# Kernel optimization log

Hardware: AMD Instinct MI355X
Metric: run time of the kernel (lower is better)

Reference implementation:

```python
import jax, jax.numpy as jnp
import numpy as np

B, T, D, H = 128, 256, 1024, 1024


def setup_inputs() -> dict:
    key = jax.random.key(0)
    ks = jax.random.split(key, 6)
    s = 0.02
    return {
        "x": jax.random.normal(ks[0], (B, T, D), dtype=jnp.float32),
        "mask": jnp.ones((B, T), dtype=jnp.float32),
        "Wi_f": jax.random.normal(ks[1], (3 * H, D), dtype=jnp.float32) * s,
        "Wh_f": jax.random.normal(ks[2], (3 * H, H), dtype=jnp.float32) * s,
        "bi_f": jnp.zeros((3 * H,), dtype=jnp.float32),
        "bh_f": jnp.zeros((3 * H,), dtype=jnp.float32),
        "Wi_r": jax.random.normal(ks[3], (3 * H, D), dtype=jnp.float32) * s,
        "Wh_r": jax.random.normal(ks[4], (3 * H, H), dtype=jnp.float32) * s,
        "bi_r": jnp.zeros((3 * H,), dtype=jnp.float32),
        "bh_r": jnp.zeros((3 * H,), dtype=jnp.float32),
    }


def _gru_scan(x_tbd, m_tb, Wi, Wh, bi, bh):
    # x_tbd: [T,B,D], m_tb: [T,B]; returns all hidden states [T,B,H]
    h0 = jnp.zeros((x_tbd.shape[1], Wh.shape[1]), dtype=x_tbd.dtype)

    def step(h, inp):
        x_t, m_t = inp
        gi = x_t @ Wi.T + bi          # [B,3H]
        gh = h @ Wh.T + bh            # [B,3H]
        i_r, i_z, i_n = jnp.split(gi, 3, axis=-1)
        h_r, h_z, h_n = jnp.split(gh, 3, axis=-1)
        r = jax.nn.sigmoid(i_r + h_r)
        z = jax.nn.sigmoid(i_z + h_z)
        n = jnp.tanh(i_n + r * h_n)
        h_new = (1.0 - z) * n + z * h
        m = m_t[:, None]
        h_out = m * h_new + (1.0 - m) * h  # masked carry-over
        return h_out, h_out

    _, hs = jax.lax.scan(step, h0, (x_tbd, m_tb))
    return hs


def reference(x, mask, Wi_f, Wh_f, bi_f, bh_f, Wi_r, Wh_r, bi_r, bh_r):
    x_t = jnp.transpose(x, (1, 0, 2))   # [T,B,D]
    m_t = jnp.transpose(mask, (1, 0))   # [T,B]
    hs_f = _gru_scan(x_t, m_t, Wi_f, Wh_f, bi_f, bh_f)              # forward in time
    hs_r = _gru_scan(x_t[::-1], m_t[::-1], Wi_r, Wh_r, bi_r, bh_r)  # reverse in time
    hs_r = hs_r[::-1]
    out = jnp.concatenate([hs_f, hs_r], axis=-1)  # [T,B,2H]
    return jnp.transpose(out, (1, 0, 2))          # [B,T,2H]
```

## Files before the change

kernel.cpp:

```cpp
#include <hip/hip_runtime.h>
#include <hip/hip_bf16.h>

typedef __hip_bfloat16 bf16;
typedef __attribute__((ext_vector_type(8))) short bf16x8;
typedef __attribute__((ext_vector_type(4))) float f32x4;

#define GLDS16(g, l)                                                  \
  __builtin_amdgcn_global_load_lds(                                   \
      (const __attribute__((address_space(1))) void*)(g),             \
      (__attribute__((address_space(3))) void*)(l), 16, 0, 0)

__device__ __forceinline__ float bf2f(bf16 v) { return __bfloat162float(v); }
__device__ __forceinline__ short f2bf(float f) {
  bf16 b = __float2bfloat16(f);
  return *reinterpret_cast<short*>(&b);
}

__device__ __forceinline__ unsigned long long ald64(const void* p) {
  return __hip_atomic_load((const unsigned long long*)p, __ATOMIC_RELAXED,
                           __HIP_MEMORY_SCOPE_AGENT);
}
__device__ __forceinline__ void ast32(void* p, unsigned v) {
  __hip_atomic_store((unsigned*)p, v, __ATOMIC_RELAXED,
                     __HIP_MEMORY_SCOPE_AGENT);
}
__device__ __forceinline__ unsigned ald32(const void* p) {
  return __hip_atomic_load((const unsigned*)p, __ATOMIC_RELAXED,
                           __HIP_MEMORY_SCOPE_AGENT);
}

__global__ __launch_bounds__(256) void cvt_bf16(const float* __restrict__ in,
                                                bf16* __restrict__ out, int n) {
  const int i = (blockIdx.x * 256 + threadIdx.x) * 8;
  if (i >= n) return;
  const float4 u = *(const float4*)(in + i);
  const float4 v = *(const float4*)(in + i + 4);
  bf16x8 w;
  w[0] = f2bf(u.x); w[1] = f2bf(u.y); w[2] = f2bf(u.z); w[3] = f2bf(u.w);
  w[4] = f2bf(v.x); w[5] = f2bf(v.y); w[6] = f2bf(v.z); w[7] = f2bf(v.w);
  *(bf16x8*)(out + i) = w;
}

__global__ __launch_bounds__(256) void cvt_whb(const float* __restrict__ Wh_f,
                                               const float* __restrict__ Wh_r,
                                               bf16* __restrict__ Whb) {
  const int t = blockIdx.x * 256 + threadIdx.x;
  const int d = t / 393216;
  int r = t % 393216;
  const int cg = r / 6144;  r %= 6144;
  const int g = r / 2048;   r %= 2048;
  const int kk = r / 64;
  const int lane = r & 63;
  const float* Wh = d ? Wh_r : Wh_f;
  const int row = g * 1024 + cg * 16 + (lane & 15);
  const int col = kk * 32 + (lane >> 4) * 8;
  const float* s = Wh + (size_t)row * 1024 + col;
  const float4 u = *(const float4*)s;
  const float4 v = *(const float4*)(s + 4);
  bf16x8 w;
  w[0] = f2bf(u.x); w[1] = f2bf(u.y); w[2] = f2bf(u.z); w[3] = f2bf(u.w);
  w[4] = f2bf(v.x); w[5] = f2bf(v.y); w[6] = f2bf(v.z); w[7] = f2bf(v.w);
  *(bf16x8*)(Whb + (size_t)t * 8) = w;
}

__global__ __launch_bounds__(256) void gi_gemm(const bf16* __restrict__ X,
                                               const bf16* __restrict__ Wi,
                                               const float* __restrict__ bi,
                                               bf16* __restrict__ Gi) {
  __shared__ bf16 As[128 * 32];
  __shared__ bf16 Bs[128 * 32];
  const int tid = threadIdx.x;
  const int lane = tid & 63;
  const int w = tid >> 6;
  const int wm = w >> 1, wn = w & 1;
  const int m0 = blockIdx.y * 128;
  const int n0 = blockIdx.x * 128;
  const int rA = lane & 15;
  const int kl = (lane >> 4) * 8;

  f32x4 acc[4][4] = {};

  const bf16* Ab = X + (size_t)m0 * 1024;
  const bf16* Bb = Wi + (size_t)n0 * 1024;

  const int arow = tid >> 2;
  const int akk = (tid & 3) * 8;

  for (int kt = 0; kt < 1024; kt += 32) {
#pragma unroll
    for (int i = 0; i < 2; ++i) {
      GLDS16(Ab + (size_t)(i * 64 + arow) * 1024 + kt + akk,
             As + (i * 256 + w * 64) * 8);
      GLDS16(Bb + (size_t)(i * 64 + arow) * 1024 + kt + akk,
             Bs + (i * 256 + w * 64) * 8);
    }
    asm volatile("s_waitcnt vmcnt(0)" ::: "memory");
    __syncthreads();

    bf16x8 a[4], b[4];
#pragma unroll
    for (int f = 0; f < 4; ++f) {
      a[f] = *(const bf16x8*)(As + (wm * 64 + f * 16 + rA) * 32 + kl);
      b[f] = *(const bf16x8*)(Bs + (wn * 64 + f * 16 + rA) * 32 + kl);
    }
#pragma unroll
    for (int mf = 0; mf < 4; ++mf)
#pragma unroll
      for (int nf = 0; nf < 4; ++nf)
        acc[mf][nf] = __builtin_amdgcn_mfma_f32_16x16x32_bf16(
            a[mf], b[nf], acc[mf][nf], 0, 0, 0);
    __syncthreads();
  }

  const int rgrp = (lane >> 4) * 4;
#pragma unroll
  for (int nf = 0; nf < 4; ++nf) {
    const int col = n0 + wn * 64 + nf * 16 + rA;
    const float bv = bi[col];
#pragma unroll
    for (int mf = 0; mf < 4; ++mf) {
#pragma unroll
      for (int j = 0; j < 4; ++j) {
        const int row = m0 + wm * 64 + mf * 16 + rgrp + j;
        Gi[(size_t)row * 3072 + col] = __float2bfloat16(acc[mf][nf][j] + bv);
      }
    }
  }
}

__global__ __launch_bounds__(256, 1) void gru_persist_s(
    const bf16* __restrict__ Whb, const float* __restrict__ bh_f,
    const float* __restrict__ bh_r, const bf16* __restrict__ Gi,
    const float* __restrict__ mask, bf16* __restrict__ h16,
    unsigned* __restrict__ flags, float* __restrict__ out) {
  __shared__ bf16 hs[32 * 1024];
  const int tid = threadIdx.x;
  const int lane = tid & 63;
  const int w = tid >> 6;
  const int mg = w >> 1;
  const int cg = w & 1;
  const int ct = blockIdx.x;
  const int bt = blockIdx.y;
  const int dir = blockIdx.z;
  unsigned* gflags = flags + (dir * 4 + bt) * 128;

  const float* bh = dir ? bh_r : bh_f;
  const bf16* gi = Gi + (size_t)dir * (32768ull * 3072ull);
  const int bt0 = bt * 32;
  const int rA = lane & 15;
  const int klane = lane >> 4;
  const int row = mg * 16 + rA;
  const int colg = ct * 32 + cg * 16 + rA;

  bf16* hbuf0 = h16 + (size_t)(dir * 2 + 0) * 131072;
  bf16* hbuf1 = h16 + (size_t)(dir * 2 + 1) * 131072;

  const bf16* bp = Whb + (size_t)dir * 3145728 +
                   (size_t)((ct * 2 + cg) * 3) * 16384 + lane * 8;
  bf16x8 br[32], bz[32];
#pragma unroll
  for (int kk = 0; kk < 32; ++kk) br[kk] = *(const bf16x8*)(bp + kk * 512);
#pragma unroll
  for (int kk = 0; kk < 32; ++kk)
    bz[kk] = *(const bf16x8*)(bp + 16384 + kk * 512);
  const bf16* bpn = bp + 32768;

  const float bhr = bh[colg];
  const float bhz = bh[1024 + colg];
  const float bhn = bh[2048 + colg];

  float hp[4] = {0.f, 0.f, 0.f, 0.f};
  const int brow0 = bt0 + mg * 16 + klane * 4;

  float gir[4], giz[4], gin[4], mk4[4];
  {
    const int time0 = dir ? 255 : 0;
#pragma unroll
    for (int j = 0; j < 4; ++j) {
      const size_t gbase = ((size_t)(brow0 + j) * 256 + time0) * 3072 + colg;
      gir[j] = bf2f(gi[gbase]);
      giz[j] = bf2f(gi[gbase + 1024]);
      gin[j] = bf2f(gi[gbase + 2048]);
      mk4[j] = mask[(brow0 + j) * 256 + time0];
    }
  }

  for (int t = 0; t < 256; ++t) {
    const int time = dir ? (255 - t) : t;
    bf16* hin = (t & 1) ? hbuf1 : hbuf0;
    bf16* hout = (t & 1) ? hbuf0 : hbuf1;

#pragma unroll
    for (int half = 0; half < 2; ++half) {
      unsigned long long vv[16];
#pragma unroll
      for (int q = 0; q < 16; ++q) {
        const int idx = (half * 16 + q) * 256 + tid;
        const int r = idx >> 8;
        const int c8 = idx & 255;
        vv[q] = ald64(hin + ((size_t)(bt0 + r) << 10) + c8 * 4);
      }
#pragma unroll
      for (int q = 0; q < 16; ++q) {
        const int idx = (half * 16 + q) * 256 + tid;
        const int r = idx >> 8;
        const int c8 = idx & 255;
        const int sw = (((c8 >> 1) ^ (r & 7)) << 4) | ((c8 & 1) << 3);
        *(unsigned long long*)((char*)hs + r * 2048 + sw) = vv[q];
      }
    }
    __syncthreads();

    f32x4 acc0 = {}, acc1 = {}, acc2 = {};
#pragma unroll
    for (int kk = 0; kk < 32; ++kk) {
      const int cidx = kk * 4 + klane;
      bf16x8 a = *(const bf16x8*)(hs + row * 1024 + ((cidx ^ (row & 7)) << 3));
      bf16x8 bn = *(const bf16x8*)(bpn + kk * 512);
      acc0 = __builtin_amdgcn_mfma_f32_16x16x32_bf16(a, br[kk], acc0, 0, 0, 0);
      acc1 = __builtin_amdgcn_mfma_f32_16x16x32_bf16(a, bz[kk], acc1, 0, 0, 0);
      acc2 = __builtin_amdgcn_mfma_f32_16x16x32_bf16(a, bn, acc2, 0, 0, 0);
    }

    float hnv[4];
#pragma unroll
    for (int j = 0; j < 4; ++j) {
      const float gr = acc0[j] + bhr + gir[j];
      const float gz = acc1[j] + bhz + giz[j];
      const float ghn = acc2[j] + bhn;
      const float r = 1.f / (1.f + __expf(-gr));
      const float z = 1.f / (1.f + __expf(-gz));
      const float nin = gin[j] + r * ghn;
      const float n = 1.f - 2.f / (__expf(2.f * nin) + 1.f);
      float hn = (1.f - z) * n + z * hp[j];
      hn = mk4[j] * hn + (1.f - mk4[j]) * hp[j];
      hp[j] = hn;
      hnv[j] = hn;
      const unsigned short hb = (unsigned short)f2bf(hn);
      const unsigned nb = (unsigned)__shfl_xor((int)hb, 1);
      if (!(lane & 1))
        ast32(hout + (((size_t)brow0 + j) << 10) + colg,
              (unsigned)hb | (nb << 16));
    }

    asm volatile("s_waitcnt vmcnt(0)" ::: "memory");
    __syncthreads();
    if (tid == 0) ast32(&gflags[ct], (unsigned)(t + 1));

#pragma unroll
    for (int j = 0; j < 4; ++j)
      out[(((size_t)(brow0 + j)) * 256 + time) * 2048 + (size_t)(dir * 1024) +
          colg] = hnv[j];

    if (t < 255) {
      const int tn = dir ? (254 - t) : (t + 1);
#pragma unroll
      for (int j = 0; j < 4; ++j) {
        const size_t gbase = ((size_t)(brow0 + j) * 256 + tn) * 3072 + colg;
        gir[j] = bf2f(gi[gbase]);
        giz[j] = bf2f(gi[gbase + 1024]);
        gin[j] = bf2f(gi[gbase + 2048]);
        mk4[j] = mask[(brow0 + j) * 256 + tn];
      }
      if (w == 0) {
        unsigned v;
        do {
          __builtin_amdgcn_s_sleep(1);
          v = ald32(&gflags[lane & 31]);
        } while (__any((int)(v < (unsigned)(t + 1))));
      }
      __builtin_amdgcn_sched_barrier(0);
      __syncthreads();
    }
  }
}

extern "C" void kernel_launch(void* const* d_in, const int* in_sizes, int n_in,
                              void* d_out, int out_size, void* d_ws,
                              size_t ws_size, hipStream_t stream) {
  const float* x = (const float*)d_in[0];
  const float* mask = (const float*)d_in[1];
  const float* Wi_f = (const float*)d_in[2];
  const float* Wh_f = (const float*)d_in[3];
  const float* bi_f = (const float*)d_in[4];
  const float* bh_f = (const float*)d_in[5];
  const float* Wi_r = (const float*)d_in[6];
  const float* Wh_r = (const float*)d_in[7];
  const float* bi_r = (const float*)d_in[8];
  const float* bh_r = (const float*)d_in[9];
  float* out = (float*)d_out;

  char* ws = (char*)d_ws;
  const size_t GI_ELEMS = 32768ull * 3072ull;
  bf16* Gi = (bf16*)ws;
  bf16* Whb = (bf16*)(ws + 2 * GI_ELEMS * sizeof(bf16));
  bf16* h16 = Whb + 2 * 3145728;
  unsigned* flags = (unsigned*)((char*)h16 + 1048576);

  bf16* Xb = (bf16*)d_out;
  bf16* Wib_f = Xb + 33554432;
  bf16* Wib_r = Wib_f + 3145728;

  hipMemsetAsync(h16, 0, 1048576 + 4096, stream);

  cvt_bf16<<<16384, 256, 0, stream>>>(x, Xb, 33554432);
  cvt_bf16<<<1536, 256, 0, stream>>>(Wi_f, Wib_f, 3145728);
  cvt_bf16<<<1536, 256, 0, stream>>>(Wi_r, Wib_r, 3145728);
  cvt_whb<<<3072, 256, 0, stream>>>(Wh_f, Wh_r, Whb);

  gi_gemm<<<dim3(24, 256), 256, 0, stream>>>(Xb, Wib_f, bi_f, Gi);
  gi_gemm<<<dim3(24, 256), 256, 0, stream>>>(Xb, Wib_r, bi_r, Gi + GI_ELEMS);

  gru_persist_s<<<dim3(32, 4, 2), 256, 0, stream>>>(Whb, bh_f, bh_r, Gi, mask,
                                                    h16, flags, out);
}
```

Before: 2.480 ms.

## Read hidden state directly into MFMA fragments from a tiled global layout

The persistent GRU kernel stops staging the full 32x1024 hidden-state slab through LDS each step. Each wave now loads its own A fragments straight from global memory with a double-buffered issue/consume pipeline interleaved with the MFMAs. The hidden-state buffer is re-laid-out into per-block 32x32 tiles so these fragment loads are contiguous. The cross-block flag wait moves to the top of the step and every wave polls it, which drops the LDS barriers. Each wave now issues more global traffic per step, and correctness depends on every wave observing the flags before it reads.

```diff
diff --git a/kernel.cpp b/kernel.cpp
--- a/kernel.cpp
+++ b/kernel.cpp
@@ -28,6 +28,11 @@
   return __hip_atomic_load((const unsigned*)p, __ATOMIC_RELAXED,
                            __HIP_MEMORY_SCOPE_AGENT);
 }
+
+union U2 {
+  unsigned long long q[2];
+  bf16x8 v;
+};
 
 __global__ __launch_bounds__(256) void cvt_bf16(const float* __restrict__ in,
                                                 bf16* __restrict__ out, int n) {
@@ -128,12 +133,11 @@
   }
 }
 
-__global__ __launch_bounds__(256, 1) void gru_persist_s(
+__global__ __launch_bounds__(256, 1) void gru_persist_d(
     const bf16* __restrict__ Whb, const float* __restrict__ bh_f,
     const float* __restrict__ bh_r, const bf16* __restrict__ Gi,
     const float* __restrict__ mask, bf16* __restrict__ h16,
     unsigned* __restrict__ flags, float* __restrict__ out) {
-  __shared__ bf16 hs[32 * 1024];
   const int tid = threadIdx.x;
   const int lane = tid & 63;
   const int w = tid >> 6;
@@ -149,11 +153,10 @@
   const int bt0 = bt * 32;
   const int rA = lane & 15;
   const int klane = lane >> 4;
-  const int row = mg * 16 + rA;
   const int colg = ct * 32 + cg * 16 + rA;
 
-  bf16* hbuf0 = h16 + (size_t)(dir * 2 + 0) * 131072;
-  bf16* hbuf1 = h16 + (size_t)(dir * 2 + 1) * 131072;
+  bf16* hb0 = h16 + (size_t)(dir * 2 + 0) * 131072;
+  bf16* hb1 = h16 + (size_t)(dir * 2 + 1) * 131072;
 
   const bf16* bp = Whb + (size_t)dir * 3145728 +
                    (size_t)((ct * 2 + cg) * 3) * 16384 + lane * 8;
@@ -171,6 +174,9 @@
 
   float hp[4] = {0.f, 0.f, 0.f, 0.f};
   const int brow0 = bt0 + mg * 16 + klane * 4;
+
+  const int fro = (mg * 16 + rA) * 32 + klane * 8;
+  const size_t slab = (size_t)(bt * 32 + ct) * 1024;
 
   float gir[4], giz[4], gin[4], mk4[4];
   {
@@ -185,42 +191,57 @@
     }
   }
 
+#define ISSUE(A, g)                                                       \
+  {                                                                       \
+    _Pragma("unroll") for (int c = 0; c < 4; ++c) {                       \
+      const bf16* p_ = cbase + (size_t)((g) * 4 + c) * 1024;              \
+      A[2 * c] = ald64(p_);                                               \
+      A[2 * c + 1] = ald64(p_ + 4);                                       \
+    }                                                                     \
+  }
+#define CONSUME(A, g)                                                     \
+  {                                                                       \
+    _Pragma("unroll") for (int c = 0; c < 4; ++c) {                       \
+      const int k_ = (g) * 4 + c;                                         \
+      U2 u_;                                                              \
+      u_.q[0] = A[2 * c];                                                 \
+      u_.q[1] = A[2 * c + 1];                                             \
+      bf16x8 bn_ = *(const bf16x8*)(bpn + k_ * 512);                      \
+      acc0 = __builtin_amdgcn_mfma_f32_16x16x32_bf16(u_.v, br[k_], acc0,  \
+                                                     0, 0, 0);            \
+      acc1 = __builtin_amdgcn_mfma_f32_16x16x32_bf16(u_.v, bz[k_], acc1,  \
+                                                     0, 0, 0);            \
+      acc2 = __builtin_amdgcn_mfma_f32_16x16x32_bf16(u_.v, bn_, acc2,     \
+                                                     0, 0, 0);            \
+    }                                                                     \
+  }
+
   for (int t = 0; t < 256; ++t) {
     const int time = dir ? (255 - t) : t;
-    bf16* hin = (t & 1) ? hbuf1 : hbuf0;
-    bf16* hout = (t & 1) ? hbuf0 : hbuf1;
-
-#pragma unroll
-    for (int half = 0; half < 2; ++half) {
-      unsigned long long vv[16];
-#pragma unroll
-      for (int q = 0; q < 16; ++q) {
-        const int idx = (half * 16 + q) * 256 + tid;
-        const int r = idx >> 8;
-        const int c8 = idx & 255;
-        vv[q] = ald64(hin + ((size_t)(bt0 + r) << 10) + c8 * 4);
-      }
-#pragma unroll
-      for (int q = 0; q < 16; ++q) {
-        const int idx = (half * 16 + q) * 256 + tid;
-        const int r = idx >> 8;
-        const int c8 = idx & 255;
-        const int sw = (((c8 >> 1) ^ (r & 7)) << 4) | ((c8 & 1) << 3);
-        *(unsigned long long*)((char*)hs + r * 2048 + sw) = vv[q];
-      }
-    }
-    __syncthreads();
-
+    const bf16* hin = (t & 1) ? hb1 : hb0;
+    bf16* hout = (t & 1) ? hb0 : hb1;
+
+    if (t > 0) {
+      unsigned v;
+      do {
+        __builtin_amdgcn_s_sleep(1);
+        v = ald32(&gflags[lane & 31]);
+      } while (__any((int)(v < (unsigned)t)));
+      __builtin_amdgcn_sched_barrier(0);
+    }
+
+    const bf16* cbase = hin + (size_t)(bt * 32) * 1024 + fro;
     f32x4 acc0 = {}, acc1 = {}, acc2 = {};
-#pragma unroll
-    for (int kk = 0; kk < 32; ++kk) {
-      const int cidx = kk * 4 + klane;
-      bf16x8 a = *(const bf16x8*)(hs + row * 1024 + ((cidx ^ (row & 7)) << 3));
-      bf16x8 bn = *(const bf16x8*)(bpn + kk * 512);
-      acc0 = __builtin_amdgcn_mfma_f32_16x16x32_bf16(a, br[kk], acc0, 0, 0, 0);
-      acc1 = __builtin_amdgcn_mfma_f32_16x16x32_bf16(a, bz[kk], acc1, 0, 0, 0);
-      acc2 = __builtin_amdgcn_mfma_f32_16x16x32_bf16(a, bn, acc2, 0, 0, 0);
-    }
+    unsigned long long a0[8], a1[8];
+    ISSUE(a0, 0);
+    ISSUE(a1, 1); CONSUME(a0, 0);
+    ISSUE(a0, 2); CONSUME(a1, 1);
+    ISSUE(a1, 3); CONSUME(a0, 2);
+    ISSUE(a0, 4); CONSUME(a1, 3);
+    ISSUE(a1, 5); CONSUME(a0, 4);
+    ISSUE(a0, 6); CONSUME(a1, 5);
+    ISSUE(a1, 7); CONSUME(a0, 6);
+    CONSUME(a1, 7);
 
     float hnv[4];
 #pragma unroll
@@ -238,9 +259,11 @@
       hnv[j] = hn;
       const unsigned short hb = (unsigned short)f2bf(hn);
       const unsigned nb = (unsigned)__shfl_xor((int)hb, 1);
-      if (!(lane & 1))
-        ast32(hout + (((size_t)brow0 + j) << 10) + colg,
-              (unsigned)hb | (nb << 16));
+      if (!(lane & 1)) {
+        const int row32 = mg * 16 + klane * 4 + j;
+        const int col32 = cg * 16 + rA;
+        ast32(hout + slab + row32 * 32 + col32, (unsigned)hb | (nb << 16));
+      }
     }
 
     asm volatile("s_waitcnt vmcnt(0)" ::: "memory");
@@ -262,17 +285,10 @@
         gin[j] = bf2f(gi[gbase + 2048]);
         mk4[j] = mask[(brow0 + j) * 256 + tn];
       }
-      if (w == 0) {
-        unsigned v;
-        do {
-          __builtin_amdgcn_s_sleep(1);
-          v = ald32(&gflags[lane & 31]);
-        } while (__any((int)(v < (unsigned)(t + 1))));
-      }
-      __builtin_amdgcn_sched_barrier(0);
-      __syncthreads();
-    }
-  }
+    }
+  }
+#undef ISSUE
+#undef CONSUME
 }
 
 extern "C" void kernel_launch(void* const* d_in, const int* in_sizes, int n_in,
@@ -311,6 +327,6 @@
   gi_gemm<<<dim3(24, 256), 256, 0, stream>>>(Xb, Wib_f, bi_f, Gi);
   gi_gemm<<<dim3(24, 256), 256, 0, stream>>>(Xb, Wib_r, bi_r, Gi + GI_ELEMS);
 
-  gru_persist_s<<<dim3(32, 4, 2), 256, 0, stream>>>(Whb, bh_f, bh_r, Gi, mask,
+  gru_persist_d<<<dim3(32, 4, 2), 256, 0, stream>>>(Whb, bh_f, bh_r, Gi, mask,
                                                     h16, flags, out);
 }
```

Result: slower. 3.787 ms (+52.7%).

## Fuse x bf16 conversion into gi_gemm and exchange hidden state via output buffer

Applied to the files above, without the earlier changes.

Removes the separate x-to-bf16 conversion pass by loading fp32 x directly in gi_gemm and converting while staging into LDS. The recurrent kernel no longer keeps a double-buffered bf16 hidden-state scratch. Each step reads the previous hidden state as fp32 from the output tensor and writes its new state straight to the output with atomic stores, with the flag wait moved to the start of the step. This saves an x-sized conversion round trip and the duplicate hidden/output stores. In exchange it doubles the bytes of hidden state read per step, and A-tile loads in the GEMM become synchronous register loads instead of direct-to-LDS loads.

```diff
diff --git a/kernel.cpp b/kernel.cpp
--- a/kernel.cpp
+++ b/kernel.cpp
@@ -16,10 +16,6 @@
   return *reinterpret_cast<short*>(&b);
 }
 
-__device__ __forceinline__ unsigned long long ald64(const void* p) {
-  return __hip_atomic_load((const unsigned long long*)p, __ATOMIC_RELAXED,
-                           __HIP_MEMORY_SCOPE_AGENT);
-}
 __device__ __forceinline__ void ast32(void* p, unsigned v) {
   __hip_atomic_store((unsigned*)p, v, __ATOMIC_RELAXED,
                      __HIP_MEMORY_SCOPE_AGENT);
@@ -63,7 +59,7 @@
   *(bf16x8*)(Whb + (size_t)t * 8) = w;
 }
 
-__global__ __launch_bounds__(256) void gi_gemm(const bf16* __restrict__ X,
+__global__ __launch_bounds__(256) void gi_gemm(const float* __restrict__ X,
                                                const bf16* __restrict__ Wi,
                                                const float* __restrict__ bi,
                                                bf16* __restrict__ Gi) {
@@ -80,7 +76,7 @@
 
   f32x4 acc[4][4] = {};
 
-  const bf16* Ab = X + (size_t)m0 * 1024;
+  const float* Ab = X + (size_t)m0 * 1024;
   const bf16* Bb = Wi + (size_t)n0 * 1024;
 
   const int arow = tid >> 2;
@@ -88,11 +84,21 @@
 
   for (int kt = 0; kt < 1024; kt += 32) {
 #pragma unroll
-    for (int i = 0; i < 2; ++i) {
-      GLDS16(Ab + (size_t)(i * 64 + arow) * 1024 + kt + akk,
-             As + (i * 256 + w * 64) * 8);
+    for (int i = 0; i < 2; ++i)
       GLDS16(Bb + (size_t)(i * 64 + arow) * 1024 + kt + akk,
              Bs + (i * 256 + w * 64) * 8);
+#pragma unroll
+    for (int i = 0; i < 2; ++i) {
+      const int c = i * 256 + tid;
+      const int row = c >> 2;
+      const int kk = (c & 3) * 8;
+      const float* sa = Ab + (size_t)row * 1024 + kt + kk;
+      const float4 a0 = *(const float4*)sa;
+      const float4 a1 = *(const float4*)(sa + 4);
+      bf16x8 av;
+      av[0] = f2bf(a0.x); av[1] = f2bf(a0.y); av[2] = f2bf(a0.z); av[3] = f2bf(a0.w);
+      av[4] = f2bf(a1.x); av[5] = f2bf(a1.y); av[6] = f2bf(a1.z); av[7] = f2bf(a1.w);
+      *(bf16x8*)(As + c * 8) = av;
     }
     asm volatile("s_waitcnt vmcnt(0)" ::: "memory");
     __syncthreads();
@@ -128,11 +134,11 @@
   }
 }
 
-__global__ __launch_bounds__(256, 1) void gru_persist_s(
+__global__ __launch_bounds__(256, 1) void gru_persist_o(
     const bf16* __restrict__ Whb, const float* __restrict__ bh_f,
     const float* __restrict__ bh_r, const bf16* __restrict__ Gi,
-    const float* __restrict__ mask, bf16* __restrict__ h16,
-    unsigned* __restrict__ flags, float* __restrict__ out) {
+    const float* __restrict__ mask, const float* __restrict__ zbuf,
+    unsigned* __restrict__ flags, float* out) {
   __shared__ bf16 hs[32 * 1024];
   const int tid = threadIdx.x;
   const int lane = tid & 63;
@@ -152,9 +158,6 @@
   const int row = mg * 16 + rA;
   const int colg = ct * 32 + cg * 16 + rA;
 
-  bf16* hbuf0 = h16 + (size_t)(dir * 2 + 0) * 131072;
-  bf16* hbuf1 = h16 + (size_t)(dir * 2 + 1) * 131072;
-
   const bf16* bp = Whb + (size_t)dir * 3145728 +
                    (size_t)((ct * 2 + cg) * 3) * 16384 + lane * 8;
   bf16x8 br[32], bz[32];
@@ -187,26 +190,48 @@
 
   for (int t = 0; t < 256; ++t) {
     const int time = dir ? (255 - t) : t;
-    bf16* hin = (t & 1) ? hbuf1 : hbuf0;
-    bf16* hout = (t & 1) ? hbuf0 : hbuf1;
-
+
+    if (t > 0) {
+      if (w == 0) {
+        unsigned v;
+        do {
+          __builtin_amdgcn_s_sleep(1);
+          v = ald32(&gflags[lane & 31]);
+        } while (__any((int)(v < (unsigned)t)));
+      }
+      __builtin_amdgcn_sched_barrier(0);
+      __syncthreads();
+      asm volatile("" ::: "memory");
+    }
+
+    const int tm = dir ? (256 - t) : (t - 1);
+    const float* hsrc0 =
+        (t == 0) ? zbuf
+                 : out + (size_t)tm * 2048 + dir * 1024 + (size_t)bt0 * 524288;
+    const size_t rstride = (t == 0) ? 1024 : 524288;
 #pragma unroll
     for (int half = 0; half < 2; ++half) {
-      unsigned long long vv[16];
-#pragma unroll
-      for (int q = 0; q < 16; ++q) {
-        const int idx = (half * 16 + q) * 256 + tid;
-        const int r = idx >> 8;
-        const int c8 = idx & 255;
-        vv[q] = ald64(hin + ((size_t)(bt0 + r) << 10) + c8 * 4);
-      }
-#pragma unroll
-      for (int q = 0; q < 16; ++q) {
-        const int idx = (half * 16 + q) * 256 + tid;
-        const int r = idx >> 8;
-        const int c8 = idx & 255;
-        const int sw = (((c8 >> 1) ^ (r & 7)) << 4) | ((c8 & 1) << 3);
-        *(unsigned long long*)((char*)hs + r * 2048 + sw) = vv[q];
+      float4 va[8], vb[8];
+#pragma unroll
+      for (int q = 0; q < 8; ++q) {
+        const int idx = (half * 8 + q) * 256 + tid;
+        const int r = idx >> 7;
+        const int ch = idx & 127;
+        const float* p = hsrc0 + (size_t)r * rstride + ch * 8;
+        va[q] = *(const float4*)p;
+        vb[q] = *(const float4*)(p + 4);
+      }
+#pragma unroll
+      for (int q = 0; q < 8; ++q) {
+        const int idx = (half * 8 + q) * 256 + tid;
+        const int r = idx >> 7;
+        const int ch = idx & 127;
+        bf16x8 wv;
+        wv[0] = f2bf(va[q].x); wv[1] = f2bf(va[q].y);
+        wv[2] = f2bf(va[q].z); wv[3] = f2bf(va[q].w);
+        wv[4] = f2bf(vb[q].x); wv[5] = f2bf(vb[q].y);
+        wv[6] = f2bf(vb[q].z); wv[7] = f2bf(vb[q].w);
+        *(bf16x8*)((char*)hs + r * 2048 + ((ch ^ (r & 7)) << 4)) = wv;
       }
     }
     __syncthreads();
@@ -222,7 +247,6 @@
       acc2 = __builtin_amdgcn_mfma_f32_16x16x32_bf16(a, bn, acc2, 0, 0, 0);
     }
 
-    float hnv[4];
 #pragma unroll
     for (int j = 0; j < 4; ++j) {
       const float gr = acc0[j] + bhr + gir[j];
@@ -235,22 +259,14 @@
       float hn = (1.f - z) * n + z * hp[j];
       hn = mk4[j] * hn + (1.f - mk4[j]) * hp[j];
       hp[j] = hn;
-      hnv[j] = hn;
-      const unsigned short hb = (unsigned short)f2bf(hn);
-      const unsigned nb = (unsigned)__shfl_xor((int)hb, 1);
-      if (!(lane & 1))
-        ast32(hout + (((size_t)brow0 + j) << 10) + colg,
-              (unsigned)hb | (nb << 16));
+      ast32(out + ((size_t)(brow0 + j) * 256 + time) * 2048 +
+                (size_t)(dir * 1024) + colg,
+            __float_as_uint(hn));
     }
 
     asm volatile("s_waitcnt vmcnt(0)" ::: "memory");
     __syncthreads();
     if (tid == 0) ast32(&gflags[ct], (unsigned)(t + 1));
-
-#pragma unroll
-    for (int j = 0; j < 4; ++j)
-      out[(((size_t)(brow0 + j)) * 256 + time) * 2048 + (size_t)(dir * 1024) +
-          colg] = hnv[j];
 
     if (t < 255) {
       const int tn = dir ? (254 - t) : (t + 1);
@@ -262,15 +278,6 @@
         gin[j] = bf2f(gi[gbase + 2048]);
         mk4[j] = mask[(brow0 + j) * 256 + tn];
       }
-      if (w == 0) {
-        unsigned v;
-        do {
-          __builtin_amdgcn_s_sleep(1);
-          v = ald32(&gflags[lane & 31]);
-        } while (__any((int)(v < (unsigned)(t + 1))));
-      }
-      __builtin_amdgcn_sched_barrier(0);
-      __syncthreads();
     }
   }
 }
@@ -293,24 +300,22 @@
   char* ws = (char*)d_ws;
   const size_t GI_ELEMS = 32768ull * 3072ull;
   bf16* Gi = (bf16*)ws;
-  bf16* Whb = (bf16*)(ws + 2 * GI_ELEMS * sizeof(bf16));
-  bf16* h16 = Whb + 2 * 3145728;
-  unsigned* flags = (unsigned*)((char*)h16 + 1048576);
-
-  bf16* Xb = (bf16*)d_out;
-  bf16* Wib_f = Xb + 33554432;
-  bf16* Wib_r = Wib_f + 3145728;
-
-  hipMemsetAsync(h16, 0, 1048576 + 4096, stream);
-
-  cvt_bf16<<<16384, 256, 0, stream>>>(x, Xb, 33554432);
+  bf16* Wreg = (bf16*)(ws + 2 * GI_ELEMS * sizeof(bf16));
+  float* zbuf = (float*)((char*)Wreg + 2 * 3145728 * sizeof(bf16));
+  unsigned* flags = (unsigned*)((char*)zbuf + 131072);
+
+  hipMemsetAsync(zbuf, 0, 131072 + 4096, stream);
+
+  bf16* Wib_f = Wreg;
+  bf16* Wib_r = Wreg + 3145728;
   cvt_bf16<<<1536, 256, 0, stream>>>(Wi_f, Wib_f, 3145728);
   cvt_bf16<<<1536, 256, 0, stream>>>(Wi_r, Wib_r, 3145728);
-  cvt_whb<<<3072, 256, 0, stream>>>(Wh_f, Wh_r, Whb);
-
-  gi_gemm<<<dim3(24, 256), 256, 0, stream>>>(Xb, Wib_f, bi_f, Gi);
-  gi_gemm<<<dim3(24, 256), 256, 0, stream>>>(Xb, Wib_r, bi_r, Gi + GI_ELEMS);
-
-  gru_persist_s<<<dim3(32, 4, 2), 256, 0, stream>>>(Whb, bh_f, bh_r, Gi, mask,
-                                                    h16, flags, out);
-}
+
+  gi_gemm<<<dim3(24, 256), 256, 0, stream>>>(x, Wib_f, bi_f, Gi);
+  gi_gemm<<<dim3(24, 256), 256, 0, stream>>>(x, Wib_r, bi_r, Gi + GI_ELEMS);
+
+  cvt_whb<<<3072, 256, 0, stream>>>(Wh_f, Wh_r, Wreg);
+
+  gru_persist_o<<<dim3(32, 4, 2), 256, 0, stream>>>(Wreg, bh_f, bh_r, Gi,
+                                                    mask, zbuf, flags, out);
+}
```

New measurement: 4.597 ms. 1.85x slower.
